# Optimization experiments

Hardware: AMD Instinct MI355X
Metric: run time of the kernel (lower is better)

Reference implementation:

```python
import jax, jax.numpy as jnp
import numpy as np

B, T, D, A = 32, 4096, 512, 64


def setup_inputs() -> dict:
    key = jax.random.key(0)
    k_x, k_m, k_w1, k_b1, k_w2 = jax.random.split(key, 5)
    x = jax.random.normal(k_x, (B, T, D), dtype=jnp.float32)
    mask = jax.random.randint(k_m, (B, T), 0, 2) > 0
    mask = mask.at[:, 0].set(True)  # guarantee >=1 valid step per row
    # params of attention MLP: Linear(D->A) with bias, Linear(A->1) no bias
    W1 = jax.random.normal(k_w1, (A, D), dtype=jnp.float32) / np.sqrt(D)
    b1 = jax.random.normal(k_b1, (A,), dtype=jnp.float32) * 0.01
    w2 = jax.random.normal(k_w2, (A,), dtype=jnp.float32) / np.sqrt(A)
    return {"x": x, "mask": mask, "W1": W1, "b1": b1, "w2": w2}


def reference(x, mask, W1, b1, w2):
    h = jnp.tanh(jnp.einsum('btd,ad->bta', x, W1) + b1)
    scores = jnp.einsum('bta,a->bt', h, w2)
    scores = jnp.where(mask, scores, -jnp.inf)
    weights = jax.nn.softmax(scores, axis=-1)          # (B, T)
    context = jnp.einsum('bt,btd->bd', weights, x)     # (B, D)
    return context, weights
```

## Files before the change

kernel.cpp:

```cpp
#include <hip/hip_runtime.h>
#include <math.h>

#define NB 32
#define NT 4096
#define ND 512
#define NA 64
#define ND4 (ND / 4)
#define RPB 128
#define NBLK (NB * NT / RPB)
#define NPW (NT / RPB)

typedef __attribute__((ext_vector_type(8))) short short8;
typedef __attribute__((ext_vector_type(4))) float f32x4;

__device__ __forceinline__ uint cvtpk(float f0, float f1) {
    uint r;
    asm("v_cvt_pk_bf16_f32 %0, %1, %2" : "=v"(r) : "v"(f0), "v"(f1));
    return r;
}
__device__ __forceinline__ void split2(float f0, float f1, uint& hw, uint& lw) {
    hw = cvtpk(f0, f1);
    float r0 = f0 - __uint_as_float(hw << 16);
    float r1 = f1 - __uint_as_float(hw & 0xffff0000u);
    lw = cvtpk(r0, r1);
}
__device__ __forceinline__ void split8(float4 a, float4 b, short8& hi, short8& lo) {
    union U { short8 s; uint u[4]; } H, L;
    split2(a.x, a.y, H.u[0], L.u[0]);
    split2(a.z, a.w, H.u[1], L.u[1]);
    split2(b.x, b.y, H.u[2], L.u[2]);
    split2(b.z, b.w, H.u[3], L.u[3]);
    hi = H.s; lo = L.s;
}

__device__ __forceinline__ float fast_tanh(float z) {
    z = fminf(fmaxf(z, -15.f), 15.f);
    float t = __expf(2.f * z);
    return (t - 1.f) * __builtin_amdgcn_rcpf(t + 1.f);
}

__global__ __launch_bounds__(256) void k_prep(
    const float* __restrict__ W1, short8* __restrict__ whi, short8* __restrict__ wlo)
{
    int t = blockIdx.x * 256 + threadIdx.x;
    int l  = t & 63;
    int nt = (t >> 6) & 3;
    int ks = t >> 8;
    int a  = nt * 16 + (l & 15);
    int kb = ks * 32 + (l >> 4) * 8;
    const float* p = W1 + a * ND + kb;
    float4 u = *(const float4*)p;
    float4 v = *(const float4*)(p + 4);
    short8 hi, lo;
    split8(u, v, hi, lo);
    whi[t] = hi;
    wlo[t] = lo;
}

__global__ __launch_bounds__(256, 4) void k_fused(
    const float* __restrict__ x, const int* __restrict__ mask,
    const short8* __restrict__ whi, const short8* __restrict__ wlo,
    const float* __restrict__ b1, const float* __restrict__ w2,
    float* __restrict__ escore, float* __restrict__ pctx, float* __restrict__ pden)
{
    __shared__ float ctxl[4][ND];
    __shared__ float wlx[4];

    const int tid = threadIdx.x;
    const int wv  = tid >> 6;
    const int l   = tid & 63;
    const int lr  = l & 15;
    const int lq  = l >> 4;
    const size_t row0 = (size_t)blockIdx.x * RPB + (size_t)wv * 32;

    const float4* __restrict__ x4 = reinterpret_cast<const float4*>(x);
    const float* xb = x + (row0 + lr) * ND + lq * 8;

    float w2v[4], b1v[4];
#pragma unroll
    for (int nt = 0; nt < 4; ++nt) {
        w2v[nt] = w2[nt * 16 + lr];
        b1v[nt] = b1[nt * 16 + lr];
    }

    f32x4 acc[2][4];
#pragma unroll
    for (int mt = 0; mt < 2; ++mt)
#pragma unroll
        for (int nt = 0; nt < 4; ++nt) acc[mt][nt] = (f32x4)0.f;

    for (int ks = 0; ks < 16; ++ks) {
        short8 ahi[2], alo[2];
#pragma unroll
        for (int mt = 0; mt < 2; ++mt) {
            const float* p = xb + mt * 16 * ND + ks * 32;
            float4 u = *(const float4*)p;
            float4 v = *(const float4*)(p + 4);
            split8(u, v, ahi[mt], alo[mt]);
        }
#pragma unroll
        for (int nt = 0; nt < 4; ++nt) {
            short8 bh = whi[(ks * 4 + nt) * 64 + l];
            short8 bl = wlo[(ks * 4 + nt) * 64 + l];
#pragma unroll
            for (int mt = 0; mt < 2; ++mt) {
                acc[mt][nt] = __builtin_amdgcn_mfma_f32_16x16x32_bf16(ahi[mt], bh, acc[mt][nt], 0, 0, 0);
                acc[mt][nt] = __builtin_amdgcn_mfma_f32_16x16x32_bf16(ahi[mt], bl, acc[mt][nt], 0, 0, 0);
                acc[mt][nt] = __builtin_amdgcn_mfma_f32_16x16x32_bf16(alo[mt], bh, acc[mt][nt], 0, 0, 0);
            }
        }
    }

    float ev[2][4];
#pragma unroll
    for (int mt = 0; mt < 2; ++mt) {
#pragma unroll
        for (int rg = 0; rg < 4; ++rg) {
            float s = 0.f;
#pragma unroll
            for (int nt = 0; nt < 4; ++nt)
                s += w2v[nt] * fast_tanh(acc[mt][nt][rg] + b1v[nt]);
            s += __shfl_xor(s, 1);
            s += __shfl_xor(s, 2);
            s += __shfl_xor(s, 4);
            s += __shfl_xor(s, 8);
            int ridx = mt * 16 + lq * 4 + rg;
            bool valid = (mask[row0 + ridx] != 0);
            float e = valid ? __expf(s) : 0.f;
            if (lr == 0) escore[row0 + ridx] = e;
            ev[mt][rg] = e;
        }
    }

    float wl = (ev[0][0] + ev[0][1]) + (ev[0][2] + ev[0][3])
             + (ev[1][0] + ev[1][1]) + (ev[1][2] + ev[1][3]);
    wl += __shfl_xor(wl, 16);
    wl += __shfl_xor(wl, 32);
    if (l == 0) wlx[wv] = wl;

    float4 ca = {0.f, 0.f, 0.f, 0.f}, cb = {0.f, 0.f, 0.f, 0.f};
#pragma unroll
    for (int t = 0; t < 32; ++t) {
        float e = __shfl(ev[t >> 4][t & 3], ((t >> 2) & 3) * 16);
        float4 xa = x4[(row0 + t) * ND4 + l];
        float4 xv = x4[(row0 + t) * ND4 + 64 + l];
        ca.x = fmaf(e, xa.x, ca.x);
        ca.y = fmaf(e, xa.y, ca.y);
        ca.z = fmaf(e, xa.z, ca.z);
        ca.w = fmaf(e, xa.w, ca.w);
        cb.x = fmaf(e, xv.x, cb.x);
        cb.y = fmaf(e, xv.y, cb.y);
        cb.z = fmaf(e, xv.z, cb.z);
        cb.w = fmaf(e, xv.w, cb.w);
    }

    *(float4*)&ctxl[wv][4 * l]       = ca;
    *(float4*)&ctxl[wv][256 + 4 * l] = cb;
    __syncthreads();

    float s0 = (ctxl[0][tid] + ctxl[1][tid]) + (ctxl[2][tid] + ctxl[3][tid]);
    int t2 = tid + 256;
    float s1 = (ctxl[0][t2] + ctxl[1][t2]) + (ctxl[2][t2] + ctxl[3][t2]);
    pctx[(size_t)blockIdx.x * ND + tid] = s0;
    pctx[(size_t)blockIdx.x * ND + t2]  = s1;
    if (tid == 0)
        pden[blockIdx.x] = (wlx[0] + wlx[1]) + (wlx[2] + wlx[3]);
}

__global__ __launch_bounds__(256) void k_merge(
    const float* __restrict__ pctx, const float* __restrict__ pden,
    float* __restrict__ ctx, float* __restrict__ invden)
{
    int b = blockIdx.x, tid = threadIdx.x;
    float denom = 0.f;
    for (int i = 0; i < NPW; ++i) denom += pden[b * NPW + i];
    float inv = 1.f / denom;
    int d0 = 2 * tid;
    float a0 = 0.f, a1 = 0.f;
    for (int i = 0; i < NPW; ++i) {
        a0 += pctx[(size_t)(b * NPW + i) * ND + d0];
        a1 += pctx[(size_t)(b * NPW + i) * ND + d0 + 1];
    }
    ctx[(size_t)b * ND + d0]     = a0 * inv;
    ctx[(size_t)b * ND + d0 + 1] = a1 * inv;
    if (tid == 0) invden[b] = inv;
}

__global__ __launch_bounds__(256) void k_weights(
    const float* __restrict__ escore, const float* __restrict__ invden,
    float* __restrict__ weights)
{
    int i = blockIdx.x * 256 + threadIdx.x;
    int b = i >> 12;
    weights[i] = escore[i] * invden[b];
}

extern "C" void kernel_launch(void* const* d_in, const int* in_sizes, int n_in,
                              void* d_out, int out_size, void* d_ws, size_t ws_size,
                              hipStream_t stream)
{
    const float* x    = (const float*)d_in[0];
    const int*   mask = (const int*)d_in[1];
    const float* W1   = (const float*)d_in[2];
    const float* b1   = (const float*)d_in[3];
    const float* w2   = (const float*)d_in[4];

    float* ctx     = (float*)d_out;
    float* weights = (float*)d_out + NB * ND;

    float* ws      = (float*)d_ws;
    float* escore  = ws;
    float* pctx    = ws + NB * NT;
    float* pden    = pctx + (size_t)NBLK * ND;
    float* invden  = pden + NBLK;
    short8* whi    = (short8*)(invden + NB);
    short8* wlo    = whi + 16 * 4 * 64;

    k_prep<<<16, 256, 0, stream>>>(W1, whi, wlo);
    k_fused<<<NBLK, 256, 0, stream>>>(x, mask, whi, wlo, b1, w2,
                                      escore, pctx, pden);
    k_merge<<<NB, 256, 0, stream>>>(pctx, pden, ctx, invden);
    k_weights<<<NB * NT / 256, 256, 0, stream>>>(escore, invden, weights);
}
```

Baseline: 95.99 us.

## Software-pipeline x loads in GEMM loop and merge tail kernels into one

In the fused kernel, the loads of x for the next K-step are issued before the current step's bf16 split and MFMAs, so global-load latency is hidden behind compute. The loop is kept rolled and occupancy is pinned with amdgpu_waves_per_eu. The merge and weights kernels are combined into a single launch: the weight blocks recompute the per-batch denominator from the partials instead of waiting on a separate merge pass. This removes one kernel launch and dependency at the cost of redundant denominator sums and an extra wrapped load on the last iteration.

Measured after the change: 102.4 us. +6.7%, slower.

```diff
diff --git a/kernel.cpp b/kernel.cpp
--- a/kernel.cpp
+++ b/kernel.cpp
@@ -57,7 +57,9 @@
     wlo[t] = lo;
 }
 
-__global__ __launch_bounds__(256, 4) void k_fused(
+__global__ void __launch_bounds__(256)
+__attribute__((amdgpu_waves_per_eu(4, 4)))
+k_fused(
     const float* __restrict__ x, const int* __restrict__ mask,
     const short8* __restrict__ whi, const short8* __restrict__ wlo,
     const float* __restrict__ b1, const float* __restrict__ w2,
@@ -74,7 +76,8 @@
     const size_t row0 = (size_t)blockIdx.x * RPB + (size_t)wv * 32;
 
     const float4* __restrict__ x4 = reinterpret_cast<const float4*>(x);
-    const float* xb = x + (row0 + lr) * ND + lq * 8;
+    const float* xb0 = x + (row0 + lr) * ND + lq * 8;
+    const float* xb1 = xb0 + 16 * ND;
 
     float w2v[4], b1v[4];
 #pragma unroll
@@ -89,26 +92,34 @@
 #pragma unroll
         for (int nt = 0; nt < 4; ++nt) acc[mt][nt] = (f32x4)0.f;
 
+    float4 cu0 = *(const float4*)(xb0);
+    float4 cv0 = *(const float4*)(xb0 + 4);
+    float4 cu1 = *(const float4*)(xb1);
+    float4 cv1 = *(const float4*)(xb1 + 4);
+
+#pragma unroll 1
     for (int ks = 0; ks < 16; ++ks) {
-        short8 ahi[2], alo[2];
-#pragma unroll
-        for (int mt = 0; mt < 2; ++mt) {
-            const float* p = xb + mt * 16 * ND + ks * 32;
-            float4 u = *(const float4*)p;
-            float4 v = *(const float4*)(p + 4);
-            split8(u, v, ahi[mt], alo[mt]);
-        }
+        const int kn = ((ks + 1) & 15) * 32;
+        float4 nu0 = *(const float4*)(xb0 + kn);
+        float4 nv0 = *(const float4*)(xb0 + kn + 4);
+        float4 nu1 = *(const float4*)(xb1 + kn);
+        float4 nv1 = *(const float4*)(xb1 + kn + 4);
+
+        short8 ahi0, alo0, ahi1, alo1;
+        split8(cu0, cv0, ahi0, alo0);
+        split8(cu1, cv1, ahi1, alo1);
 #pragma unroll
         for (int nt = 0; nt < 4; ++nt) {
             short8 bh = whi[(ks * 4 + nt) * 64 + l];
             short8 bl = wlo[(ks * 4 + nt) * 64 + l];
-#pragma unroll
-            for (int mt = 0; mt < 2; ++mt) {
-                acc[mt][nt] = __builtin_amdgcn_mfma_f32_16x16x32_bf16(ahi[mt], bh, acc[mt][nt], 0, 0, 0);
-                acc[mt][nt] = __builtin_amdgcn_mfma_f32_16x16x32_bf16(ahi[mt], bl, acc[mt][nt], 0, 0, 0);
-                acc[mt][nt] = __builtin_amdgcn_mfma_f32_16x16x32_bf16(alo[mt], bh, acc[mt][nt], 0, 0, 0);
-            }
+            acc[0][nt] = __builtin_amdgcn_mfma_f32_16x16x32_bf16(ahi0, bh, acc[0][nt], 0, 0, 0);
+            acc[0][nt] = __builtin_amdgcn_mfma_f32_16x16x32_bf16(ahi0, bl, acc[0][nt], 0, 0, 0);
+            acc[0][nt] = __builtin_amdgcn_mfma_f32_16x16x32_bf16(alo0, bh, acc[0][nt], 0, 0, 0);
+            acc[1][nt] = __builtin_amdgcn_mfma_f32_16x16x32_bf16(ahi1, bh, acc[1][nt], 0, 0, 0);
+            acc[1][nt] = __builtin_amdgcn_mfma_f32_16x16x32_bf16(ahi1, bl, acc[1][nt], 0, 0, 0);
+            acc[1][nt] = __builtin_amdgcn_mfma_f32_16x16x32_bf16(alo1, bh, acc[1][nt], 0, 0, 0);
         }
+        cu0 = nu0; cv0 = nv0; cu1 = nu1; cv1 = nv1;
     }
 
     float ev[2][4];
@@ -167,32 +178,32 @@
         pden[blockIdx.x] = (wlx[0] + wlx[1]) + (wlx[2] + wlx[3]);
 }
 
-__global__ __launch_bounds__(256) void k_merge(
+__global__ __launch_bounds__(256) void k_tail(
     const float* __restrict__ pctx, const float* __restrict__ pden,
-    float* __restrict__ ctx, float* __restrict__ invden)
-{
-    int b = blockIdx.x, tid = threadIdx.x;
-    float denom = 0.f;
-    for (int i = 0; i < NPW; ++i) denom += pden[b * NPW + i];
-    float inv = 1.f / denom;
-    int d0 = 2 * tid;
-    float a0 = 0.f, a1 = 0.f;
-    for (int i = 0; i < NPW; ++i) {
-        a0 += pctx[(size_t)(b * NPW + i) * ND + d0];
-        a1 += pctx[(size_t)(b * NPW + i) * ND + d0 + 1];
-    }
-    ctx[(size_t)b * ND + d0]     = a0 * inv;
-    ctx[(size_t)b * ND + d0 + 1] = a1 * inv;
-    if (tid == 0) invden[b] = inv;
-}
-
-__global__ __launch_bounds__(256) void k_weights(
-    const float* __restrict__ escore, const float* __restrict__ invden,
-    float* __restrict__ weights)
-{
-    int i = blockIdx.x * 256 + threadIdx.x;
-    int b = i >> 12;
-    weights[i] = escore[i] * invden[b];
+    const float* __restrict__ escore,
+    float* __restrict__ ctx, float* __restrict__ weights)
+{
+    int bid = blockIdx.x, tid = threadIdx.x;
+    if (bid < NB) {
+        int b = bid;
+        float denom = 0.f;
+        for (int i = 0; i < NPW; ++i) denom += pden[b * NPW + i];
+        float inv = 1.f / denom;
+        int d0 = 2 * tid;
+        float a0 = 0.f, a1 = 0.f;
+        for (int i = 0; i < NPW; ++i) {
+            a0 += pctx[(size_t)(b * NPW + i) * ND + d0];
+            a1 += pctx[(size_t)(b * NPW + i) * ND + d0 + 1];
+        }
+        ctx[(size_t)b * ND + d0]     = a0 * inv;
+        ctx[(size_t)b * ND + d0 + 1] = a1 * inv;
+    } else {
+        int i = (bid - NB) * 256 + tid;
+        int b = i >> 12;
+        float denom = 0.f;
+        for (int j = 0; j < NPW; ++j) denom += pden[b * NPW + j];
+        weights[i] = escore[i] * (1.f / denom);
+    }
 }
 
 extern "C" void kernel_launch(void* const* d_in, const int* in_sizes, int n_in,
@@ -212,13 +223,12 @@
     float* escore  = ws;
     float* pctx    = ws + NB * NT;
     float* pden    = pctx + (size_t)NBLK * ND;
-    float* invden  = pden + NBLK;
-    short8* whi    = (short8*)(invden + NB);
+    short8* whi    = (short8*)(pden + NBLK);
     short8* wlo    = whi + 16 * 4 * 64;
 
     k_prep<<<16, 256, 0, stream>>>(W1, whi, wlo);
     k_fused<<<NBLK, 256, 0, stream>>>(x, mask, whi, wlo, b1, w2,
                                       escore, pctx, pden);
-    k_merge<<<NB, 256, 0, stream>>>(pctx, pden, ctx, invden);
-    k_weights<<<NB * NT / 256, 256, 0, stream>>>(escore, invden, weights);
-}
+    k_tail<<<NB + NB * NT / 256, 256, 0, stream>>>(pctx, pden, escore,
+                                                   ctx, weights);
+}
```
